# Optimization experiments

Measured on AMD Instinct MI355X. Metric: run time of the kernel, lower is better.

## Reference

```python
import jax, jax.numpy as jnp
import numpy as np
import math

B, S, HID = 2, 2048, 512
NH, NKV, HD = 8, 2, 256
ROT = 64          # partial_rotary_factor 0.25 * head_dim 256
ROPE_THETA = 10000000.0
EPS = 1e-6


def _rms_norm(x, w):
    # zero-centered RMSNorm: x / rms * (1 + w)
    rms = jnp.sqrt(jnp.mean(x * x, axis=-1, keepdims=True) + EPS)
    return x / rms * (1.0 + w)


def _partial_rope(x, cos, sin):
    # x: [B,S,H,HD]; cos/sin: [S, ROT//2]
    xr = x[..., :ROT].reshape(*x.shape[:-1], ROT // 2, 2)
    a, b = xr[..., 0], xr[..., 1]
    c = cos[None, :, None, :]
    s = sin[None, :, None, :]
    rot = jnp.stack([a * c - b * s, a * s + b * c], axis=-1).reshape(*x.shape[:-1], ROT)
    return jnp.concatenate([rot, x[..., ROT:]], axis=-1)


def setup_inputs() -> dict:
    key = jax.random.key(0)
    ks = jax.random.split(key, 6)
    x = jax.random.normal(ks[0], (B, S, HID), dtype=jnp.float32)
    # real RoPE frequencies
    inv_freq = 1.0 / (ROPE_THETA ** (np.arange(0, ROT, 2, dtype=np.float32) / ROT))
    t = np.arange(S, dtype=np.float32)
    angles = np.outer(t, inv_freq)  # [S, ROT//2]
    cos = jnp.asarray(np.cos(angles), dtype=jnp.float32)
    sin = jnp.asarray(np.sin(angles), dtype=jnp.float32)
    # additive causal mask [S,S]
    mask = jnp.where(jnp.tril(jnp.ones((S, S), dtype=bool)), 0.0, -1e9).astype(jnp.float32)
    sc = 0.02
    wq = jax.random.normal(ks[1], (HID, NH * HD), dtype=jnp.float32) * sc
    wk = jax.random.normal(ks[2], (HID, NKV * HD), dtype=jnp.float32) * sc
    wv = jax.random.normal(ks[3], (HID, NKV * HD), dtype=jnp.float32) * sc
    wo = jax.random.normal(ks[4], (NH * HD, HID), dtype=jnp.float32) * sc
    q_norm_w = jnp.zeros((HD,), dtype=jnp.float32)
    k_norm_w = jnp.zeros((HD,), dtype=jnp.float32)
    return {"x": x, "cos": cos, "sin": sin, "mask": mask,
            "wq": wq, "wk": wk, "wv": wv, "wo": wo,
            "q_norm_w": q_norm_w, "k_norm_w": k_norm_w}


def reference(x, cos, sin, mask, wq, wk, wv, wo, q_norm_w, k_norm_w):
    b, s, _ = x.shape
    groups = NH // NKV
    q = (x @ wq).reshape(b, s, NH, HD)
    k = (x @ wk).reshape(b, s, NKV, HD)
    v = (x @ wv).reshape(b, s, NKV, HD)
    q = _partial_rope(_rms_norm(q, q_norm_w), cos, sin)
    k = _partial_rope(_rms_norm(k, k_norm_w), cos, sin)
    # GQA: broadcast kv heads to NH
    k = jnp.repeat(k, groups, axis=2)  # [b,s,NH,HD]
    v = jnp.repeat(v, groups, axis=2)
    scale = math.sqrt(HD)
    scores = jnp.einsum('bqhd,bkhd->bhqk', q, k) / scale
    scores = scores + mask[None, None, :, :]
    attn = jax.nn.softmax(scores, axis=-1)
    out = jnp.einsum('bhqk,bkhd->bqhd', attn, v).reshape(b, s, NH * HD)
    return out @ wo
```

## Files before the change

### kernel.cpp

```cpp
#include <hip/hip_runtime.h>

#define S_LEN 2048
#define NHQ 8
#define NKV 2
#define HD 256
#define KVB 32

typedef __attribute__((ext_vector_type(8))) short bf16x8;
typedef __attribute__((ext_vector_type(4))) short bf16x4;
typedef __attribute__((ext_vector_type(4))) float f32x4;
typedef __attribute__((ext_vector_type(16))) float f32x16;
typedef __attribute__((ext_vector_type(4))) unsigned u32x4;

__device__ __forceinline__ short f2bf(float f) {
    unsigned u = __builtin_bit_cast(unsigned, f);
    u += 0x7FFFu + ((u >> 16) & 1u);
    return (short)(u >> 16);
}
__device__ __forceinline__ float bf2f(short s) {
    unsigned u = ((unsigned)(unsigned short)s) << 16;
    return __builtin_bit_cast(float, u);
}
__device__ __forceinline__ unsigned cvtpk(float a, float b) {
    unsigned r;
    asm("v_cvt_pk_bf16_f32 %0, %1, %2" : "=v"(r) : "v"(a), "v"(b));
    return r;
}
__device__ __forceinline__ void gload16(const short* g, short* l) {
    __builtin_amdgcn_global_load_lds((const __attribute__((address_space(1))) unsigned*)g,
                                     (__attribute__((address_space(3))) unsigned*)l, 16, 0, 0);
}
__device__ __forceinline__ float bperm(int srclane, float v) {
    return __builtin_bit_cast(float,
        __builtin_amdgcn_ds_bpermute(srclane * 4, __builtin_bit_cast(int, v)));
}

__global__ __launch_bounds__(256) void cvt_kernel(const float* __restrict__ in,
                                                  short* __restrict__ out, int n) {
    int i = (blockIdx.x * 256 + threadIdx.x) * 4;
    if (i + 3 < n) {
        float4 f = *(const float4*)(in + i);
        bf16x4 o;
        o[0] = f2bf(f.x); o[1] = f2bf(f.y); o[2] = f2bf(f.z); o[3] = f2bf(f.w);
        *(bf16x4*)(out + i) = o;
    }
}

__global__ __launch_bounds__(256) void wt_kernel(const float* __restrict__ in,
                                                 short* __restrict__ out,
                                                 int K, int N) {
    __shared__ short tile[64][72];
    int n0 = blockIdx.x * 64, k0 = blockIdx.y * 64;
    int t = threadIdx.x;
    #pragma unroll
    for (int i = 0; i < 16; i++) {
        int flat = i * 256 + t; int r = flat >> 6, c = flat & 63;
        tile[r][c] = f2bf(in[(long)(k0 + r) * N + n0 + c]);
    }
    __syncthreads();
    #pragma unroll
    for (int i = 0; i < 16; i++) {
        int flat = i * 256 + t; int r = flat >> 6, c = flat & 63;
        out[(long)(n0 + r) * K + k0 + c] = tile[c][r];
    }
}

template<int BN, int WRITE_BF16>
__global__ __launch_bounds__(256) void gemm_bt(const short* __restrict__ A,
                                               const short* __restrict__ Bt,
                                               void* __restrict__ Cv,
                                               int M, int N, int K) {
    constexpr int NI = BN / 32;
    __shared__ short As[128 * 32];
    __shared__ short Bs[BN * 32];
    const int t = threadIdx.x;
    const int lane = t & 63, w = t >> 6;
    const int lr = lane & 15, lg = lane >> 4;
    const int m0 = blockIdx.y * 128, n0 = blockIdx.x * BN;
    const int wm = (w >> 1) * 64, wn = (w & 1) * (BN / 2);

    f32x4 acc[4][NI];
    #pragma unroll
    for (int i = 0; i < 4; i++)
        #pragma unroll
        for (int j = 0; j < NI; j++) acc[i][j] = (f32x4){0.f, 0.f, 0.f, 0.f};

    for (int k0 = 0; k0 < K; k0 += 32) {
        __syncthreads();
        #pragma unroll
        for (int r = 0; r < 2; r++) {
            int sbase = r * 2048 + w * 512;
            int srow = (sbase + lane * 8) >> 5, scol = (sbase + lane * 8) & 31;
            gload16(A + (long)(m0 + srow) * K + k0 + scol, &As[sbase]);
        }
        #pragma unroll
        for (int r = 0; r < BN / 64; r++) {
            int sbase = r * 2048 + w * 512;
            int srow = (sbase + lane * 8) >> 5, scol = (sbase + lane * 8) & 31;
            gload16(Bt + (long)(n0 + srow) * K + k0 + scol, &Bs[sbase]);
        }
        __syncthreads();
        bf16x8 af[4], bfr[NI];
        #pragma unroll
        for (int mi = 0; mi < 4; mi++)
            af[mi] = *(const bf16x8*)&As[(wm + mi * 16 + lr) * 32 + lg * 8];
        #pragma unroll
        for (int ni = 0; ni < NI; ni++)
            bfr[ni] = *(const bf16x8*)&Bs[(wn + ni * 16 + lr) * 32 + lg * 8];
        #pragma unroll
        for (int mi = 0; mi < 4; mi++)
            #pragma unroll
            for (int ni = 0; ni < NI; ni++)
                acc[mi][ni] = __builtin_amdgcn_mfma_f32_16x16x32_bf16(af[mi], bfr[ni], acc[mi][ni], 0, 0, 0);
    }
    #pragma unroll
    for (int mi = 0; mi < 4; mi++)
    #pragma unroll
    for (int ni = 0; ni < NI; ni++)
    #pragma unroll
    for (int r = 0; r < 4; r++) {
        long row = m0 + wm + mi * 16 + lg * 4 + r;
        long col = n0 + wn + ni * 16 + lr;
        float v = acc[mi][ni][r];
        if (WRITE_BF16) ((short*)Cv)[row * N + col] = f2bf(v);
        else            ((float*)Cv)[row * N + col] = v;
    }
}

__global__ __launch_bounds__(256) void norm_rope_kernel(
    const short* __restrict__ in, short* __restrict__ out,
    const float* __restrict__ w, const float* __restrict__ cosb,
    const float* __restrict__ sinb, int H, long ldin, long cofs,
    long ob, long oh, long os, float scale) {
    int vec = blockIdx.x * 4 + (threadIdx.x >> 6);
    int lane = threadIdx.x & 63;
    int token = vec / H, head = vec % H;
    int b = token / S_LEN, s = token % S_LEN;

    bf16x4 xv = *(const bf16x4*)(in + (long)token * ldin + cofs + head * 256 + lane * 4);
    float x0 = bf2f(xv[0]), x1 = bf2f(xv[1]), x2 = bf2f(xv[2]), x3 = bf2f(xv[3]);
    float ss = x0 * x0 + x1 * x1 + x2 * x2 + x3 * x3;
    #pragma unroll
    for (int m = 1; m < 64; m <<= 1) ss += __shfl_xor(ss, m);
    float inv = rsqrtf(ss * (1.f / 256.f) + 1e-6f);

    float4 wv = *(const float4*)(w + lane * 4);
    float y0 = x0 * inv * (1.f + wv.x);
    float y1 = x1 * inv * (1.f + wv.y);
    float y2 = x2 * inv * (1.f + wv.z);
    float y3 = x3 * inv * (1.f + wv.w);

    if (lane < 16) {
        float2 c = *(const float2*)&cosb[s * 32 + lane * 2];
        float2 sn = *(const float2*)&sinb[s * 32 + lane * 2];
        float a0 = y0 * c.x - y1 * sn.x, b0 = y0 * sn.x + y1 * c.x;
        float a1 = y2 * c.y - y3 * sn.y, b1 = y2 * sn.y + y3 * c.y;
        y0 = a0; y1 = b0; y2 = a1; y3 = b1;
    }
    y0 *= scale; y1 *= scale; y2 *= scale; y3 *= scale;
    long oidx = (long)b * ob + (long)head * oh + (long)s * os + lane * 4;
    bf16x4 o; o[0] = f2bf(y0); o[1] = f2bf(y1); o[2] = f2bf(y2); o[3] = f2bf(y3);
    *(bf16x4*)(out + oidx) = o;
}

__global__ __launch_bounds__(256) void transpose_v_kernel(const short* __restrict__ C,
                                                          short* __restrict__ vr) {
    __shared__ short tile[64][65];
    int s0 = blockIdx.x * 64, d0 = blockIdx.y * 64;
    int bkv = blockIdx.z; int b = bkv >> 1, kv = bkv & 1;
    int t = threadIdx.x;
    #pragma unroll
    for (int i = 0; i < 16; i++) {
        int flat = i * 256 + t; int si = flat >> 6, di = flat & 63;
        tile[si][di] = C[(long)(b * S_LEN + s0 + si) * 3072 + 2560 + kv * 256 + d0 + di];
    }
    __syncthreads();
    #pragma unroll
    for (int i = 0; i < 16; i++) {
        int flat = i * 256 + t; int di = flat >> 6, si = flat & 63;
        vr[(long)(bkv * 256 + d0 + di) * S_LEN + s0 + si] = tile[si][di];
    }
}

__global__ __launch_bounds__(128) void flash_kernel(const short* __restrict__ Q,
                                                    const short* __restrict__ Kt,
                                                    const short* __restrict__ Vt,
                                                    short* __restrict__ O) {
    __shared__ short KsA[KVB * 256];
    __shared__ short VsA[256 * KVB];
    __shared__ short KsB[KVB * 256];
    __shared__ short VsB[256 * KVB];

    int idx = blockIdx.x;
    int qt = (idx < 256) ? (31 - (idx >> 4)) : ((idx - 256) >> 4);
    int bh = idx & 15, h = bh & 7, b = bh >> 3;
    int kv = h >> 2;
    int t = threadIdx.x, lane = t & 63, w = t >> 6;
    int ln = lane & 31, hi = lane >> 5;
    int q0 = qt * 64 + w * 32;
    int qg = q0 + ln;

    const short* Kb = Kt + (long)(b * NKV + kv) * S_LEN * HD;
    const short* Vb = Vt + (long)(b * NKV + kv) * HD * S_LEN;

    bf16x8 qf[16];
    {
        const short* qrow = Q + ((long)(b * S_LEN + qg) * NHQ + h) * HD + hi * 8;
        #pragma unroll
        for (int dc = 0; dc < 16; dc++) qf[dc] = *(const bf16x8*)&qrow[dc * 16];
    }

    f32x16 acc[8];
    #pragma unroll
    for (int i = 0; i < 8; i++)
        #pragma unroll
        for (int j = 0; j < 16; j++) acc[i][j] = 0.f;
    float m = -1e30f, l = 0.f;

    int nt = 2 * qt + 2;

    auto stage = [&](short* Ks, short* Vs, int tile) {
        int k0 = tile * KVB;
        #pragma unroll
        for (int c = 0; c < 8; c++) {
            int o = (w * 8 + c) * 1024 + lane * 16;
            int key = o >> 9, db = o & 511;
            gload16(Kb + (long)(k0 + key) * HD + ((db ^ ((key & 7) << 4)) >> 1),
                    &Ks[(w * 8 + c) * 512]);
        }
        #pragma unroll
        for (int c = 0; c < 8; c++) {
            int o = (w * 8 + c) * 1024 + lane * 16;
            int d = o >> 6, kb = o & 63;
            gload16(Vb + (long)d * S_LEN + k0 + ((kb ^ ((d & 6) << 3)) >> 1),
                    &Vs[(w * 8 + c) * 512]);
        }
    };

    auto compute = [&](const short* Ks, const short* Vs, int k0) {
        f32x16 sA, sB;
        #pragma unroll
        for (int j = 0; j < 16; j++) { sA[j] = 0.f; sB[j] = 0.f; }
        __builtin_amdgcn_s_setprio(1);
        #pragma unroll
        for (int dc = 0; dc < 16; dc += 2) {
            int kb0 = (dc * 32 + hi * 16) ^ ((ln & 7) << 4);
            int kb1 = ((dc + 1) * 32 + hi * 16) ^ ((ln & 7) << 4);
            bf16x8 kf0 = *(const bf16x8*)((const char*)Ks + ln * 512 + kb0);
            bf16x8 kf1 = *(const bf16x8*)((const char*)Ks + ln * 512 + kb1);
            sA = __builtin_amdgcn_mfma_f32_32x32x16_bf16(kf0, qf[dc],     sA, 0, 0, 0);
            sB = __builtin_amdgcn_mfma_f32_32x32x16_bf16(kf1, qf[dc + 1], sB, 0, 0, 0);
        }
        __builtin_amdgcn_s_setprio(0);
        f32x16 s;
        #pragma unroll
        for (int j = 0; j < 16; j++) s[j] = sA[j] + sB[j];

        if (k0 + KVB - 1 > q0) {
            #pragma unroll
            for (int r = 0; r < 16; r++) {
                int key_g = k0 + (r & 3) + 8 * (r >> 2) + 4 * hi;
                if (key_g > qg) s[r] = -1e30f;
            }
        }
        float mt = s[0];
        #pragma unroll
        for (int r = 1; r < 16; r++) mt = fmaxf(mt, s[r]);
        mt = fmaxf(mt, __shfl_xor(mt, 32));
        float mn = m;
        if (!__all(mt <= m + 8.f)) {
            mn = fmaxf(m, mt);
            float f = __expf(m - mn);
            m = mn;
            float fr[16];
            #pragma unroll
            for (int r = 0; r < 16; r++)
                fr[r] = bperm((r & 3) + 8 * (r >> 2) + 4 * hi, f);
            #pragma unroll
            for (int i = 0; i < 8; i++)
                #pragma unroll
                for (int r = 0; r < 16; r++) acc[i][r] *= fr[r];
            l *= f;
        }
        float p[16], ps = 0.f;
        #pragma unroll
        for (int r = 0; r < 16; r++) { p[r] = __expf(s[r] - mn); ps += p[r]; }
        ps += __shfl_xor(ps, 32);
        l += ps;

        unsigned pw[8];
        #pragma unroll
        for (int kc = 0; kc < 2; kc++) {
            unsigned X = cvtpk(p[kc * 8 + 0], p[kc * 8 + 1]);
            unsigned Y = cvtpk(p[kc * 8 + 4], p[kc * 8 + 5]);
            unsigned Z = cvtpk(p[kc * 8 + 2], p[kc * 8 + 3]);
            unsigned W = cvtpk(p[kc * 8 + 6], p[kc * 8 + 7]);
            asm volatile("v_permlane32_swap_b32 %0, %1" : "+v"(X), "+v"(Y));
            asm volatile("v_permlane32_swap_b32 %0, %1" : "+v"(Z), "+v"(W));
            pw[kc * 4 + 0] = X; pw[kc * 4 + 1] = Z;
            pw[kc * 4 + 2] = Y; pw[kc * 4 + 3] = W;
        }
        u32x4 w0v = {pw[0], pw[1], pw[2], pw[3]};
        u32x4 w1v = {pw[4], pw[5], pw[6], pw[7]};
        bf16x8 pa0 = __builtin_bit_cast(bf16x8, w0v);
        bf16x8 pa1 = __builtin_bit_cast(bf16x8, w1v);

        __builtin_amdgcn_s_setprio(1);
        #pragma unroll
        for (int db = 0; db < 8; db++) {
            int drow = db * 32 + ln;
            int sw = (drow & 6) << 3;
            bf16x8 vf0 = *(const bf16x8*)((const char*)Vs + drow * 64 + ((hi * 16) ^ sw));
            bf16x8 vf1 = *(const bf16x8*)((const char*)Vs + drow * 64 + ((32 + hi * 16) ^ sw));
            acc[db] = __builtin_amdgcn_mfma_f32_32x32x16_bf16(pa0, vf0, acc[db], 0, 0, 0);
            acc[db] = __builtin_amdgcn_mfma_f32_32x32x16_bf16(pa1, vf1, acc[db], 0, 0, 0);
        }
        __builtin_amdgcn_s_setprio(0);
    };

    #define VW16 asm volatile("s_waitcnt vmcnt(16)" ::: "memory")
    #define VW0  asm volatile("s_waitcnt vmcnt(0)" ::: "memory")
    #define BAR  __builtin_amdgcn_s_barrier()

    stage(KsA, VsA, 0);
    stage(KsB, VsB, 1);

    int tt = 0;
    for (; tt + 2 < nt; tt += 2) {
        VW16; BAR;
        if (tt * KVB <= q0 + 31) compute(KsA, VsA, tt * KVB);
        BAR;
        stage(KsA, VsA, tt + 2);
        __builtin_amdgcn_sched_barrier(0);
        VW16; BAR;
        if ((tt + 1) * KVB <= q0 + 31) compute(KsB, VsB, (tt + 1) * KVB);
        BAR;
        stage(KsB, VsB, tt + 3);
        __builtin_amdgcn_sched_barrier(0);
    }
    VW16; BAR;
    if ((nt - 2) * KVB <= q0 + 31) compute(KsA, VsA, (nt - 2) * KVB);
    VW0; BAR;
    if ((nt - 1) * KVB <= q0 + 31) compute(KsB, VsB, (nt - 1) * KVB);

    #undef VW16
    #undef VW0
    #undef BAR

    float linv = 1.f / l;
    float lr[16];
    #pragma unroll
    for (int r = 0; r < 16; r++)
        lr[r] = bperm((r & 3) + 8 * (r >> 2) + 4 * hi, linv);
    #pragma unroll
    for (int db = 0; db < 8; db++)
        #pragma unroll
        for (int r = 0; r < 16; r++) {
            int qrow = q0 + (r & 3) + 8 * (r >> 2) + 4 * hi;
            O[(long)(b * S_LEN + qrow) * 2048 + h * HD + db * 32 + ln] =
                f2bf(acc[db][r] * lr[r]);
        }
}

extern "C" void kernel_launch(void* const* d_in, const int* in_sizes, int n_in,
                              void* d_out, int out_size, void* d_ws, size_t ws_size,
                              hipStream_t stream) {
    const float* x    = (const float*)d_in[0];
    const float* cosb = (const float*)d_in[1];
    const float* sinb = (const float*)d_in[2];
    const float* wq   = (const float*)d_in[4];
    const float* wk   = (const float*)d_in[5];
    const float* wv   = (const float*)d_in[6];
    const float* wo   = (const float*)d_in[7];
    const float* qnw  = (const float*)d_in[8];
    const float* knw  = (const float*)d_in[9];
    float* out = (float*)d_out;

    char* ws = (char*)d_ws;
    short* xb   = (short*)(ws + 0);
    short* wfus = (short*)(ws + 4194304);
    short* wot  = (short*)(ws + 7340032);
    short* C    = (short*)(ws + 9437184);
    short* ao   = (short*)(ws + 9437184);
    short* qro  = (short*)(ws + 34603008);
    short* kr   = (short*)(ws + 51380224);
    short* vr   = (short*)(ws + 55574528);

    cvt_kernel<<<2048, 256, 0, stream>>>(x, xb, 2097152);
    wt_kernel<<<dim3(32, 8), 256, 0, stream>>>(wq, wfus,              512, 2048);
    wt_kernel<<<dim3(8, 8),  256, 0, stream>>>(wk, wfus + 2048 * 512, 512, 512);
    wt_kernel<<<dim3(8, 8),  256, 0, stream>>>(wv, wfus + 2560 * 512, 512, 512);
    wt_kernel<<<dim3(8, 32), 256, 0, stream>>>(wo, wot, 2048, 512);

    gemm_bt<128, 1><<<dim3(24, 32), 256, 0, stream>>>(xb, wfus, C, 4096, 3072, 512);

    norm_rope_kernel<<<8192, 256, 0, stream>>>(C, qro, qnw, cosb, sinb, 8,
                                               3072L, 0L, 4194304L, 256L, 2048L, 0.0625f);
    norm_rope_kernel<<<2048, 256, 0, stream>>>(C, kr, knw, cosb, sinb, 2,
                                               3072L, 2048L, 1048576L, 524288L, 256L, 1.0f);
    transpose_v_kernel<<<dim3(32, 4, 4), 256, 0, stream>>>(C, vr);

    flash_kernel<<<512, 128, 0, stream>>>(qro, kr, vr, ao);

    gemm_bt<64, 0><<<dim3(8, 32), 256, 0, stream>>>(ao, wot, out, 4096, 512, 2048);
}
```

Baseline: 220.0 us.

## Split KV range across wave pairs in 512-thread flash blocks with LDS merge

The flash attention kernel now uses 512-thread blocks covering 128 query rows. Each query group of 32 rows is handled by two waves that take alternating KV tiles, so the sequential KV loop per wave is roughly halved. Two tile pairs are staged per phase into a single 132 KB shared buffer. At the end the partial softmax states (acc, m, l) are merged through LDS. This trades more LDS use and a merge step for more waves per CU and a shorter per-wave critical path. It also drops the reversed heavy-first block ordering, which can leave causal-imbalanced blocks on the tail.

```diff
diff --git a/kernel.cpp b/kernel.cpp
--- a/kernel.cpp
+++ b/kernel.cpp
@@ -182,22 +182,20 @@
     }
 }
 
-__global__ __launch_bounds__(128) void flash_kernel(const short* __restrict__ Q,
-                                                    const short* __restrict__ Kt,
-                                                    const short* __restrict__ Vt,
-                                                    short* __restrict__ O) {
-    __shared__ short KsA[KVB * 256];
-    __shared__ short VsA[256 * KVB];
-    __shared__ short KsB[KVB * 256];
-    __shared__ short VsB[256 * KVB];
+__global__ __launch_bounds__(512, 2) void flash_kernel(const short* __restrict__ Q,
+                                                       const short* __restrict__ Kt,
+                                                       const short* __restrict__ Vt,
+                                                       short* __restrict__ O) {
+    __shared__ __align__(16) char smem[132096];
 
     int idx = blockIdx.x;
-    int qt = (idx < 256) ? (31 - (idx >> 4)) : ((idx - 256) >> 4);
+    int a = idx >> 4;
     int bh = idx & 15, h = bh & 7, b = bh >> 3;
     int kv = h >> 2;
     int t = threadIdx.x, lane = t & 63, w = t >> 6;
+    int g = w >> 1, p = w & 1;
     int ln = lane & 31, hi = lane >> 5;
-    int q0 = qt * 64 + w * 32;
+    int q0 = a * 128 + g * 32;
     int qg = q0 + ln;
 
     const short* Kb = Kt + (long)(b * NKV + kv) * S_LEN * HD;
@@ -217,27 +215,32 @@
         for (int j = 0; j < 16; j++) acc[i][j] = 0.f;
     float m = -1e30f, l = 0.f;
 
-    int nt = 2 * qt + 2;
-
-    auto stage = [&](short* Ks, short* Vs, int tile) {
-        int k0 = tile * KVB;
-        #pragma unroll
-        for (int c = 0; c < 8; c++) {
-            int o = (w * 8 + c) * 1024 + lane * 16;
-            int key = o >> 9, db = o & 511;
-            gload16(Kb + (long)(k0 + key) * HD + ((db ^ ((key & 7) << 4)) >> 1),
-                    &Ks[(w * 8 + c) * 512]);
-        }
-        #pragma unroll
-        for (int c = 0; c < 8; c++) {
-            int o = (w * 8 + c) * 1024 + lane * 16;
-            int d = o >> 6, kb = o & 63;
-            gload16(Vb + (long)d * S_LEN + k0 + ((kb ^ ((d & 6) << 3)) >> 1),
-                    &Vs[(w * 8 + c) * 512]);
+    const int nph  = 2 * a + 2;
+    const int Tmax = 4 * a + g;
+
+    auto stagepair = [&](int sp, int T0) {
+        #pragma unroll
+        for (int pp = 0; pp < 2; pp++) {
+            int k0s = (T0 + pp) * KVB;
+            short* Ktile = (short*)(smem + (sp * 2 + pp) * 16384);
+            short* Vtile = (short*)(smem + 65536 + (sp * 2 + pp) * 16384);
+            #pragma unroll
+            for (int c = 0; c < 2; c++) {
+                int o = c * 8192 + w * 1024 + lane * 16;
+                int key = o >> 9, db = o & 511;
+                gload16(Kb + (long)(k0s + key) * HD + ((db ^ ((key & 7) << 4)) >> 1),
+                        Ktile + (c * 8192 + w * 1024) / 2);
+                int d = o >> 6, kb = o & 63;
+                gload16(Vb + (long)d * S_LEN + k0s + ((kb ^ ((d & 6) << 3)) >> 1),
+                        Vtile + (c * 8192 + w * 1024) / 2);
+            }
         }
     };
 
-    auto compute = [&](const short* Ks, const short* Vs, int k0) {
+    auto computeT = [&](int sp, int T) {
+        const char* Ks = (const char*)smem + (sp * 2 + p) * 16384;
+        const char* Vs = (const char*)smem + 65536 + (sp * 2 + p) * 16384;
+        int k0 = T * KVB;
         f32x16 sA, sB;
         #pragma unroll
         for (int j = 0; j < 16; j++) { sA[j] = 0.f; sB[j] = 0.f; }
@@ -246,8 +249,8 @@
         for (int dc = 0; dc < 16; dc += 2) {
             int kb0 = (dc * 32 + hi * 16) ^ ((ln & 7) << 4);
             int kb1 = ((dc + 1) * 32 + hi * 16) ^ ((ln & 7) << 4);
-            bf16x8 kf0 = *(const bf16x8*)((const char*)Ks + ln * 512 + kb0);
-            bf16x8 kf1 = *(const bf16x8*)((const char*)Ks + ln * 512 + kb1);
+            bf16x8 kf0 = *(const bf16x8*)(Ks + ln * 512 + kb0);
+            bf16x8 kf1 = *(const bf16x8*)(Ks + ln * 512 + kb1);
             sA = __builtin_amdgcn_mfma_f32_32x32x16_bf16(kf0, qf[dc],     sA, 0, 0, 0);
             sB = __builtin_amdgcn_mfma_f32_32x32x16_bf16(kf1, qf[dc + 1], sB, 0, 0, 0);
         }
@@ -282,19 +285,19 @@
                 for (int r = 0; r < 16; r++) acc[i][r] *= fr[r];
             l *= f;
         }
-        float p[16], ps = 0.f;
-        #pragma unroll
-        for (int r = 0; r < 16; r++) { p[r] = __expf(s[r] - mn); ps += p[r]; }
+        float pr[16], ps = 0.f;
+        #pragma unroll
+        for (int r = 0; r < 16; r++) { pr[r] = __expf(s[r] - mn); ps += pr[r]; }
         ps += __shfl_xor(ps, 32);
         l += ps;
 
         unsigned pw[8];
         #pragma unroll
         for (int kc = 0; kc < 2; kc++) {
-            unsigned X = cvtpk(p[kc * 8 + 0], p[kc * 8 + 1]);
-            unsigned Y = cvtpk(p[kc * 8 + 4], p[kc * 8 + 5]);
-            unsigned Z = cvtpk(p[kc * 8 + 2], p[kc * 8 + 3]);
-            unsigned W = cvtpk(p[kc * 8 + 6], p[kc * 8 + 7]);
+            unsigned X = cvtpk(pr[kc * 8 + 0], pr[kc * 8 + 1]);
+            unsigned Y = cvtpk(pr[kc * 8 + 4], pr[kc * 8 + 5]);
+            unsigned Z = cvtpk(pr[kc * 8 + 2], pr[kc * 8 + 3]);
+            unsigned W = cvtpk(pr[kc * 8 + 6], pr[kc * 8 + 7]);
             asm volatile("v_permlane32_swap_b32 %0, %1" : "+v"(X), "+v"(Y));
             asm volatile("v_permlane32_swap_b32 %0, %1" : "+v"(Z), "+v"(W));
             pw[kc * 4 + 0] = X; pw[kc * 4 + 1] = Z;
@@ -310,56 +313,63 @@
         for (int db = 0; db < 8; db++) {
             int drow = db * 32 + ln;
             int sw = (drow & 6) << 3;
-            bf16x8 vf0 = *(const bf16x8*)((const char*)Vs + drow * 64 + ((hi * 16) ^ sw));
-            bf16x8 vf1 = *(const bf16x8*)((const char*)Vs + drow * 64 + ((32 + hi * 16) ^ sw));
+            bf16x8 vf0 = *(const bf16x8*)(Vs + drow * 64 + ((hi * 16) ^ sw));
+            bf16x8 vf1 = *(const bf16x8*)(Vs + drow * 64 + ((32 + hi * 16) ^ sw));
             acc[db] = __builtin_amdgcn_mfma_f32_32x32x16_bf16(pa0, vf0, acc[db], 0, 0, 0);
             acc[db] = __builtin_amdgcn_mfma_f32_32x32x16_bf16(pa1, vf1, acc[db], 0, 0, 0);
         }
         __builtin_amdgcn_s_setprio(0);
     };
 
-    #define VW16 asm volatile("s_waitcnt vmcnt(16)" ::: "memory")
-    #define VW0  asm volatile("s_waitcnt vmcnt(0)" ::: "memory")
-    #define BAR  __builtin_amdgcn_s_barrier()
-
-    stage(KsA, VsA, 0);
-    stage(KsB, VsB, 1);
-
-    int tt = 0;
-    for (; tt + 2 < nt; tt += 2) {
-        VW16; BAR;
-        if (tt * KVB <= q0 + 31) compute(KsA, VsA, tt * KVB);
-        BAR;
-        stage(KsA, VsA, tt + 2);
+    stagepair(0, 0);
+    stagepair(1, 2);
+
+    for (int ph = 0; ph < nph; ph++) {
+        int sp = ph & 1;
+        if (ph + 1 < nph) { asm volatile("s_waitcnt vmcnt(8)" ::: "memory"); }
+        else              { asm volatile("s_waitcnt vmcnt(0)" ::: "memory"); }
+        __builtin_amdgcn_s_barrier();
+        int T = 2 * ph + p;
+        if (T <= Tmax) computeT(sp, T);
+        __builtin_amdgcn_s_barrier();
+        if (ph + 2 < nph) stagepair(sp, 2 * ph + 4);
         __builtin_amdgcn_sched_barrier(0);
-        VW16; BAR;
-        if ((tt + 1) * KVB <= q0 + 31) compute(KsB, VsB, (tt + 1) * KVB);
-        BAR;
-        stage(KsB, VsB, tt + 3);
-        __builtin_amdgcn_sched_barrier(0);
-    }
-    VW16; BAR;
-    if ((nt - 2) * KVB <= q0 + 31) compute(KsA, VsA, (nt - 2) * KVB);
-    VW0; BAR;
-    if ((nt - 1) * KVB <= q0 + 31) compute(KsB, VsB, (nt - 1) * KVB);
-
-    #undef VW16
-    #undef VW0
-    #undef BAR
-
-    float linv = 1.f / l;
-    float lr[16];
-    #pragma unroll
-    for (int r = 0; r < 16; r++)
-        lr[r] = bperm((r & 3) + 8 * (r >> 2) + 4 * hi, linv);
-    #pragma unroll
-    for (int db = 0; db < 8; db++)
+    }
+
+    float* accb = (float*)smem;
+    float* mlb  = (float*)(smem + 131072);
+    if (p == 1) {
+        #pragma unroll
+        for (int db = 0; db < 8; db++)
+            #pragma unroll
+            for (int r = 0; r < 16; r++)
+                accb[g * 8192 + (db * 16 + r) * 64 + hi * 32 + ln] = acc[db][r];
+        if (hi == 0) { mlb[g * 32 + ln] = m; mlb[128 + g * 32 + ln] = l; }
+    }
+    __syncthreads();
+    if (p == 0) {
+        float m1 = mlb[g * 32 + ln], l1 = mlb[128 + g * 32 + ln];
+        float M  = fmaxf(m, m1);
+        float f0 = __expf(m - M), f1 = __expf(m1 - M);
+        float lt = l * f0 + l1 * f1;
+        float w0 = f0 / lt, w1 = f1 / lt;
+        float fr0[16], fr1[16];
         #pragma unroll
         for (int r = 0; r < 16; r++) {
-            int qrow = q0 + (r & 3) + 8 * (r >> 2) + 4 * hi;
-            O[(long)(b * S_LEN + qrow) * 2048 + h * HD + db * 32 + ln] =
-                f2bf(acc[db][r] * lr[r]);
-        }
+            int crow = (r & 3) + 8 * (r >> 2) + 4 * hi;
+            fr0[r] = bperm(crow, w0);
+            fr1[r] = bperm(crow, w1);
+        }
+        #pragma unroll
+        for (int db = 0; db < 8; db++)
+            #pragma unroll
+            for (int r = 0; r < 16; r++) {
+                float a1 = accb[g * 8192 + (db * 16 + r) * 64 + hi * 32 + ln];
+                int qrow = q0 + (r & 3) + 8 * (r >> 2) + 4 * hi;
+                O[(long)(b * S_LEN + qrow) * 2048 + h * HD + db * 32 + ln] =
+                    f2bf(acc[db][r] * fr0[r] + a1 * fr1[r]);
+            }
+    }
 }
 
 extern "C" void kernel_launch(void* const* d_in, const int* in_sizes, int n_in,
@@ -400,7 +410,7 @@
                                                3072L, 2048L, 1048576L, 524288L, 256L, 1.0f);
     transpose_v_kernel<<<dim3(32, 4, 4), 256, 0, stream>>>(C, vr);
 
-    flash_kernel<<<512, 128, 0, stream>>>(qro, kr, vr, ao);
+    flash_kernel<<<256, 512, 0, stream>>>(qro, kr, vr, ao);
 
     gemm_bt<64, 0><<<dim3(8, 32), 256, 0, stream>>>(ao, wot, out, 4096, 512, 2048);
 }
```

Result: faster. 215.6 us (-2.0%).
